# Optimization experiments

Measured on AMD Instinct MI355X. Metric: run time of the kernel, lower is better.

Reference implementation:

```python
import jax, jax.numpy as jnp
import numpy as np

H = 256  # hidden_dim
N = 500000  # num_orbitals
M = 8192  # num_molecules


def setup_inputs() -> dict:
    key = jax.random.key(0)
    ks = jax.random.split(key, 12)
    s = lambda fan_in: 1.0 / np.sqrt(fan_in)
    inp = {
        "orbital_embeddings": jax.random.normal(ks[0], (N, H), dtype=jnp.float32),
        "batch": jnp.sort(jax.random.randint(ks[1], (N,), 0, M, dtype=jnp.int32)),
        "num_molecules": M,
        # attention MLP: Linear(H, H//2) -> ReLU -> Linear(H//2, 1)
        "aW1": jax.random.uniform(ks[2], (H, H // 2), jnp.float32, -s(H), s(H)),
        "ab1": jnp.zeros((H // 2,), jnp.float32),
        "aW2": jax.random.uniform(ks[3], (H // 2, 1), jnp.float32, -s(H // 2), s(H // 2)),
        "ab2": jnp.zeros((1,), jnp.float32),
        # global head: Linear(H,H)->ReLU->Linear(H,H//2)->ReLU->Linear(H//2,1)
        "gW1": jax.random.uniform(ks[4], (H, H), jnp.float32, -s(H), s(H)),
        "gb1": jnp.zeros((H,), jnp.float32),
        "gW2": jax.random.uniform(ks[5], (H, H // 2), jnp.float32, -s(H), s(H)),
        "gb2": jnp.zeros((H // 2,), jnp.float32),
        "gW3": jax.random.uniform(ks[6], (H // 2, 1), jnp.float32, -s(H // 2), s(H // 2)),
        "gb3": jnp.zeros((1,), jnp.float32),
    }
    return inp


def reference(orbital_embeddings, batch, num_molecules, aW1, ab1, aW2, ab2,
              gW1, gb1, gW2, gb2, gW3, gb3):
    # attention logits: [N, 1] (dropout is identity in eval mode)
    h = jax.nn.relu(orbital_embeddings @ aW1 + ab1)
    logits = h @ aW2 + ab2  # [N, 1]

    # per-molecule (segment) softmax over orbitals, numerically stable
    lg = logits[:, 0]  # [N]
    seg_max = jax.ops.segment_max(lg, batch, num_segments=num_molecules)  # [M]
    seg_max = jnp.where(jnp.isfinite(seg_max), seg_max, 0.0)  # empty segments
    ex = jnp.exp(lg - seg_max[batch])  # [N]
    denom = jax.ops.segment_sum(ex, batch, num_segments=num_molecules)  # [M]
    w = ex / denom[batch]  # [N]

    # weighted scatter-add pooling -> [M, H]
    weighted = orbital_embeddings * w[:, None]
    mol = jax.ops.segment_sum(weighted, batch, num_segments=num_molecules)

    # global head MLP -> [M, 1]
    g = jax.nn.relu(mol @ gW1 + gb1)
    g = jax.nn.relu(g @ gW2 + gb2)
    return g @ gW3 + gb3
```

## Files before the change

kernel.cpp:

```cpp
#include <hip/hip_runtime.h>
#include <hip/hip_bf16.h>

#define H      256
#define CAP    64
#define GRID12 512

typedef _Float16 f16x8 __attribute__((ext_vector_type(8)));
typedef float    f32x4 __attribute__((ext_vector_type(4)));

#define AS3(p) ((__attribute__((address_space(3))) void*)(p))
#define AS1(p) ((const __attribute__((address_space(1))) void*)(p))

__global__ __launch_bounds__(256) void k0_pack(
    const float* __restrict__ aW1, const float* __restrict__ gW1,
    const float* __restrict__ gW2,
    _Float16* __restrict__ aW1F, float* __restrict__ gW1P, float* __restrict__ gW2P)
{
    int idx = blockIdx.x * 256 + threadIdx.x;
    int stride = gridDim.x * 256;
    for (int e8 = idx; e8 < 4096; e8 += stride) {
        int l = e8 & 63, kknt = e8 >> 6;
        int kk = kknt & 7, nt = kknt >> 3;
        int j = nt*16 + (l & 15);
        int kbase = kk*32 + (l >> 4)*8;
        f16x8 v;
        #pragma unroll
        for (int e = 0; e < 8; ++e) v[e] = (_Float16)aW1[(kbase + e)*128 + j];
        *reinterpret_cast<f16x8*>(aW1F + e8*8) = v;
    }
    for (int e = idx; e < 64*256*4; e += stride) {
        int s = e & 3, j = (e >> 2) & 255, kq = e >> 10;
        gW1P[e] = gW1[(kq*4+s)*256 + j];
    }
    for (int e = idx; e < 64*128*4; e += stride) {
        int s = e & 3, j = (e >> 2) & 127, kq = e >> 9;
        gW2P[e] = gW2[(kq*4+s)*128 + j];
    }
}

__global__ __launch_bounds__(256) void k2a_starts(
    const int* __restrict__ batch, int* __restrict__ starts, int N, int M)
{
    int i = blockIdx.x * 256 + threadIdx.x;
    if (i >= N) return;
    int b = batch[i];
    if (i == 0) {
        for (int m = 0; m <= b; ++m) starts[m] = 0;
    } else {
        int p = batch[i-1];
        for (int m = p + 1; m <= b; ++m) starts[m] = i;
    }
    if (i == N - 1) {
        for (int m = b + 1; m <= M; ++m) starts[m] = N;
    }
}

__global__ __launch_bounds__(256) void k12_fused(
    const float* __restrict__ emb, const int* __restrict__ starts,
    const _Float16* __restrict__ aW1F, const float* __restrict__ ab1,
    const float* __restrict__ aW2, const float* __restrict__ ab2,
    float* __restrict__ mol, int M)
{
    __shared__ __align__(16) float ef[CAP * H];
    __shared__ float pr[4][CAP];
    __shared__ float lgs[CAP];
    __shared__ float wl[CAP];

    const int t = threadIdx.x, w = t >> 6, l = t & 63;
    char* ldsb = reinterpret_cast<char*>(ef);
    const f32x4 zero = {0.f, 0.f, 0.f, 0.f};

    f16x8 bf[2][8];
    #pragma unroll
    for (int nt2 = 0; nt2 < 2; ++nt2)
        #pragma unroll
        for (int kk = 0; kk < 8; ++kk)
            bf[nt2][kk] = *reinterpret_cast<const f16x8*>(
                aW1F + (size_t)(((2*w + nt2)*8 + kk)*64 + l)*8);

    float b1v[2], w2v[2];
    #pragma unroll
    for (int nt2 = 0; nt2 < 2; ++nt2) {
        int j = 32*w + nt2*16 + (l & 15);
        b1v[nt2] = ab1[j];
        w2v[nt2] = aW2[j];
    }
    const float bo = ab2[0];

    int m = blockIdx.x, start = 0, end = 0;
    for (;;) {
        if (m >= M) return;
        start = starts[m]; end = starts[m + 1];
        if (start < end) break;
        mol[(size_t)m*H + t] = 0.f;
        m += GRID12;
    }

    int c0 = start;
    int cc = min(CAP, end - c0);
    float mx = -INFINITY, s = 0.f, acc = 0.f;

    for (;;) {
        const int  cur_m = m, cur_cc = cc;
        const bool last_chunk = (c0 + CAP >= end);

        __syncthreads();

        #pragma unroll
        for (int i = 0; i < 16; ++i) {
            int r = w*16 + i;
            if (r < cc) {
                const char* gs = reinterpret_cast<const char*>(emb + (size_t)(c0 + r)*H)
                               + ((l*16) ^ ((r & 7) << 4));
#if __has_builtin(__builtin_amdgcn_global_load_lds)
                __builtin_amdgcn_global_load_lds(AS1(gs), AS3(ldsb + r*1024), 16, 0, 0);
#else
                *reinterpret_cast<float4*>(ldsb + r*1024 + l*16) =
                    *reinterpret_cast<const float4*>(gs);
#endif
            }
        }

        int nm = m, nc0 = c0 + CAP, nend = end;
        bool have_next = true;
        if (last_chunk) {
            nm = m + GRID12;
            for (;;) {
                if (nm >= M) { have_next = false; break; }
                int ns = starts[nm], ne = starts[nm + 1];
                if (ns < ne) { nc0 = ns; nend = ne; break; }
                mol[(size_t)nm*H + t] = 0.f;
                nm += GRID12;
            }
        }
        int ncc = have_next ? min(CAP, nend - nc0) : 0;
        __syncthreads();

        const int nr = (cur_cc + 15) >> 4;
        for (int rt = 0; rt < nr; ++rt) {
            int row   = rt*16 + (l & 15);
            int rbase = row*1024 + (l >> 4)*32;
            int swz   = (row & 7) << 4;
            f32x4 a20 = zero, a21 = zero;
            #pragma unroll
            for (int kk = 0; kk < 8; ++kk) {
                int rb = rbase + kk*128;
                float4 a0 = *reinterpret_cast<const float4*>(ldsb + ( rb       ^ swz));
                float4 a1 = *reinterpret_cast<const float4*>(ldsb + ((rb + 16) ^ swz));
                f16x8 af;
                af[0]=(_Float16)a0.x; af[1]=(_Float16)a0.y; af[2]=(_Float16)a0.z; af[3]=(_Float16)a0.w;
                af[4]=(_Float16)a1.x; af[5]=(_Float16)a1.y; af[6]=(_Float16)a1.z; af[7]=(_Float16)a1.w;
                a20 = __builtin_amdgcn_mfma_f32_16x16x32_f16(af, bf[0][kk], a20, 0, 0, 0);
                a21 = __builtin_amdgcn_mfma_f32_16x16x32_f16(af, bf[1][kk], a21, 0, 0, 0);
            }
            #pragma unroll
            for (int r = 0; r < 4; ++r) {
                float h0 = a20[r] + b1v[0]; h0 = h0 > 0.f ? h0 : 0.f;
                float h1 = a21[r] + b1v[1]; h1 = h1 > 0.f ? h1 : 0.f;
                float p = h0*w2v[0] + h1*w2v[1];
                p += __shfl_xor(p, 1, 64);
                p += __shfl_xor(p, 2, 64);
                p += __shfl_xor(p, 4, 64);
                p += __shfl_xor(p, 8, 64);
                if ((l & 15) == 0) pr[w][rt*16 + (l >> 4)*4 + r] = p;
            }
        }
        __syncthreads();
        if (t < CAP) lgs[t] = pr[0][t] + pr[1][t] + pr[2][t] + pr[3][t] + bo;
        __syncthreads();

        float lg = (l < cur_cc) ? lgs[l] : -INFINITY;
        float mc = lg;
        mc = fmaxf(mc, __shfl_xor(mc, 1, 64));
        mc = fmaxf(mc, __shfl_xor(mc, 2, 64));
        mc = fmaxf(mc, __shfl_xor(mc, 4, 64));
        mc = fmaxf(mc, __shfl_xor(mc, 8, 64));
        mc = fmaxf(mc, __shfl_xor(mc, 16, 64));
        mc = fmaxf(mc, __shfl_xor(mc, 32, 64));
        float mxn = fmaxf(mx, mc);
        float rsc = __expf(mx - mxn);
        float e = (l < cur_cc) ? __expf(lg - mxn) : 0.f;
        float sc = e;
        sc += __shfl_xor(sc, 1, 64);
        sc += __shfl_xor(sc, 2, 64);
        sc += __shfl_xor(sc, 4, 64);
        sc += __shfl_xor(sc, 8, 64);
        sc += __shfl_xor(sc, 16, 64);
        sc += __shfl_xor(sc, 32, 64);
        s = s*rsc + sc;
        if (w == 0) wl[l] = e;
        mx = mxn;
        __syncthreads();

        acc *= rsc;
        #pragma unroll 4
        for (int g = 0; g < cur_cc; ++g) {
            float ev = *reinterpret_cast<const float*>(
                ldsb + ((g*1024 + t*4) ^ ((g & 7) << 4)));
            acc += wl[g] * ev;
        }

        if (last_chunk) {
            mol[(size_t)cur_m*H + t] = acc / s;
            mx = -INFINITY; s = 0.f; acc = 0.f;
        }
        if (!have_next) return;
        m = nm; c0 = nc0; end = nend; cc = ncc;
    }
}

__global__ __launch_bounds__(256) void k3_mlp(
    const float* __restrict__ mol, const float* __restrict__ gW1P,
    const float* __restrict__ gb1, const float* __restrict__ gW2P,
    const float* __restrict__ gb2, const float* __restrict__ gW3,
    const float* __restrict__ gb3, float* __restrict__ out, int M)
{
    __shared__ __align__(16) float mt[32 * 256];
    __shared__ __align__(16) float g1[32 * 256];
    __shared__ float tmp[4][16];
    int t = threadIdx.x;
    int blk = blockIdx.x;

    #pragma unroll
    for (int i = 0; i < 8; ++i) {
        int f = t + i*256;
        long gidx = (long)blk*2048 + f;
        float4 v = make_float4(0.f,0.f,0.f,0.f);
        if (gidx < (long)M*64) v = reinterpret_cast<const float4*>(mol)[gidx];
        reinterpret_cast<float4*>(mt)[f] = v;
    }
    __syncthreads();

    int j = t & 127, mh = t >> 7;

    float a0[16], a1[16];
    #pragma unroll
    for (int m = 0; m < 16; ++m) { a0[m] = 0.f; a1[m] = 0.f; }
    for (int kq = 0; kq < 64; ++kq) {
        float4 w0 = reinterpret_cast<const float4*>(gW1P)[kq*256 + j];
        float4 w1 = reinterpret_cast<const float4*>(gW1P)[kq*256 + j + 128];
        #pragma unroll
        for (int m = 0; m < 16; ++m) {
            float4 e = *reinterpret_cast<const float4*>(&mt[(mh*16 + m)*256 + kq*4]);
            a0[m] += e.x*w0.x + e.y*w0.y + e.z*w0.z + e.w*w0.w;
            a1[m] += e.x*w1.x + e.y*w1.y + e.z*w1.z + e.w*w1.w;
        }
    }
    {
        float b0 = gb1[j], b1 = gb1[j + 128];
        #pragma unroll
        for (int m = 0; m < 16; ++m) {
            float v0 = a0[m] + b0; v0 = v0 > 0.f ? v0 : 0.f;
            float v1 = a1[m] + b1; v1 = v1 > 0.f ? v1 : 0.f;
            g1[(mh*16 + m)*256 + j]       = v0;
            g1[(mh*16 + m)*256 + j + 128] = v1;
        }
    }
    __syncthreads();

    float a2[16];
    #pragma unroll
    for (int m = 0; m < 16; ++m) a2[m] = 0.f;
    for (int kq = 0; kq < 64; ++kq) {
        float4 w = reinterpret_cast<const float4*>(gW2P)[kq*128 + j];
        #pragma unroll
        for (int m = 0; m < 16; ++m) {
            float4 e = *reinterpret_cast<const float4*>(&g1[(mh*16 + m)*256 + kq*4]);
            a2[m] += e.x*w.x + e.y*w.y + e.z*w.z + e.w*w.w;
        }
    }

    float b2 = gb2[j], w3 = gW3[j];
    float p[16];
    #pragma unroll
    for (int m = 0; m < 16; ++m) {
        float v = a2[m] + b2; v = v > 0.f ? v : 0.f;
        p[m] = v * w3;
    }
    #pragma unroll
    for (int off = 32; off >= 1; off >>= 1) {
        #pragma unroll
        for (int m = 0; m < 16; ++m) p[m] += __shfl_xor(p[m], off, 64);
    }
    int wid = t >> 6;
    if ((t & 63) == 0) {
        #pragma unroll
        for (int m = 0; m < 16; ++m) tmp[wid][m] = p[m];
    }
    __syncthreads();
    if (t < 32) {
        int om = blk*32 + t;
        if (om < M) out[om] = tmp[(t >> 4)*2][t & 15] + tmp[(t >> 4)*2 + 1][t & 15] + gb3[0];
    }
}

extern "C" void kernel_launch(void* const* d_in, const int* in_sizes, int n_in,
                              void* d_out, int out_size, void* d_ws, size_t ws_size,
                              hipStream_t stream) {
    const float* emb  = (const float*)d_in[0];
    const int*   batch= (const int*)d_in[1];
    const float* aW1  = (const float*)d_in[3];
    const float* ab1  = (const float*)d_in[4];
    const float* aW2  = (const float*)d_in[5];
    const float* ab2  = (const float*)d_in[6];
    const float* gW1  = (const float*)d_in[7];
    const float* gb1  = (const float*)d_in[8];
    const float* gW2  = (const float*)d_in[9];
    const float* gb2  = (const float*)d_in[10];
    const float* gW3  = (const float*)d_in[11];
    const float* gb3  = (const float*)d_in[12];
    float* outp = (float*)d_out;

    int N = in_sizes[0] / H;
    int M = out_size;

    char* ws = (char*)d_ws;
    size_t off = 0;
    float*     mol    = (float*)(ws + off);    off += (8u<<20);
    _Float16*  aW1F   = (_Float16*)(ws + off); off += 65536;
    float*     gW1P   = (float*)(ws + off);    off += 262144;
    float*     gW2P   = (float*)(ws + off);    off += 131072;
    int*       starts = (int*)(ws + off);      off += (size_t)(M+1)*4;

    int g12 = M < GRID12 ? M : GRID12;

    k0_pack<<<64, 256, 0, stream>>>(aW1, gW1, gW2, aW1F, gW1P, gW2P);
    k2a_starts<<<(N + 255)/256, 256, 0, stream>>>(batch, starts, N, M);
    k12_fused<<<g12, 256, 0, stream>>>(emb, starts, aW1F, ab1, aW2, ab2, mol, M);
    k3_mlp<<<(M + 31)/32, 256, 0, stream>>>(mol, gW1P, gb1, gW2P, gb2, gW3, gb3, outp, M);
}
```

Measured before the change: 254.0 us.

## Double-buffer embedding chunks in LDS to prefetch the next chunk during compute

The fused attention-pool kernel now keeps two LDS buffers of 32 rows each instead of one 64-row buffer. While the current chunk is processed, the global_load_lds for the next chunk (or next molecule) is issued, and partial waits via s_waitcnt vmcnt plus raw s_barrier replace several __syncthreads. The intent is to hide global-memory latency behind the MFMA and softmax work. It also drops the separate lgs reduction step and clamps out-of-range rows to the last valid row instead of skipping them. Smaller chunks add more per-chunk barrier and softmax overhead, and the hand-placed waitcnt handling is fragile.

After: 276.2 us. 1.09x slower.

```diff
diff --git a/kernel.cpp b/kernel.cpp
--- a/kernel.cpp
+++ b/kernel.cpp
@@ -2,14 +2,21 @@
 #include <hip/hip_bf16.h>
 
 #define H      256
-#define CAP    64
+#define CAP    32
 #define GRID12 512
+#define RPW    8
 
 typedef _Float16 f16x8 __attribute__((ext_vector_type(8)));
 typedef float    f32x4 __attribute__((ext_vector_type(4)));
 
 #define AS3(p) ((__attribute__((address_space(3))) void*)(p))
 #define AS1(p) ((const __attribute__((address_space(1))) void*)(p))
+
+#define VMWAIT8() asm volatile("s_waitcnt vmcnt(8)" ::: "memory")
+#define VMWAIT0() asm volatile("s_waitcnt vmcnt(0)" ::: "memory")
+#define LGKM0()   asm volatile("s_waitcnt lgkmcnt(0)" ::: "memory")
+#define SBAR()    __builtin_amdgcn_s_barrier()
+#define SCHED0()  __builtin_amdgcn_sched_barrier(0)
 
 __global__ __launch_bounds__(256) void k0_pack(
     const float* __restrict__ aW1, const float* __restrict__ gW1,
@@ -61,13 +68,11 @@
     const float* __restrict__ aW2, const float* __restrict__ ab2,
     float* __restrict__ mol, int M)
 {
-    __shared__ __align__(16) float ef[CAP * H];
+    __shared__ __align__(16) float ef[2][CAP * H];
     __shared__ float pr[4][CAP];
-    __shared__ float lgs[CAP];
     __shared__ float wl[CAP];
 
     const int t = threadIdx.x, w = t >> 6, l = t & 63;
-    char* ldsb = reinterpret_cast<char*>(ef);
     const f32x4 zero = {0.f, 0.f, 0.f, 0.f};
 
     f16x8 bf[2][8];
@@ -98,28 +103,25 @@
 
     int c0 = start;
     int cc = min(CAP, end - c0);
+
+#define ISSUE8(BUF, C0, CC) do {                                                 \
+    char* dst_ = reinterpret_cast<char*>(ef[BUF]);                               \
+    _Pragma("unroll")                                                            \
+    for (int i_ = 0; i_ < RPW; ++i_) {                                           \
+        int r_  = w*RPW + i_;                                                    \
+        int rr_ = r_ < (CC) ? r_ : (CC) - 1;                                     \
+        const char* gs_ = reinterpret_cast<const char*>(                         \
+            emb + (size_t)((C0) + rr_)*H) + ((l*16) ^ ((rr_ & 7) << 4));         \
+        __builtin_amdgcn_global_load_lds(AS1(gs_), AS3(dst_ + r_*1024), 16, 0, 0);\
+    } } while (0)
+
+    ISSUE8(0, c0, cc);
+    int cur = 0;
     float mx = -INFINITY, s = 0.f, acc = 0.f;
 
     for (;;) {
         const int  cur_m = m, cur_cc = cc;
         const bool last_chunk = (c0 + CAP >= end);
-
-        __syncthreads();
-
-        #pragma unroll
-        for (int i = 0; i < 16; ++i) {
-            int r = w*16 + i;
-            if (r < cc) {
-                const char* gs = reinterpret_cast<const char*>(emb + (size_t)(c0 + r)*H)
-                               + ((l*16) ^ ((r & 7) << 4));
-#if __has_builtin(__builtin_amdgcn_global_load_lds)
-                __builtin_amdgcn_global_load_lds(AS1(gs), AS3(ldsb + r*1024), 16, 0, 0);
-#else
-                *reinterpret_cast<float4*>(ldsb + r*1024 + l*16) =
-                    *reinterpret_cast<const float4*>(gs);
-#endif
-            }
-        }
 
         int nm = m, nc0 = c0 + CAP, nend = end;
         bool have_next = true;
@@ -134,7 +136,19 @@
             }
         }
         int ncc = have_next ? min(CAP, nend - nc0) : 0;
-        __syncthreads();
+
+        SBAR();
+
+        if (have_next) {
+            ISSUE8(cur ^ 1, nc0, ncc);
+            VMWAIT8();
+        } else {
+            VMWAIT0();
+        }
+        SCHED0();
+        SBAR();
+
+        const char* bufb = reinterpret_cast<const char*>(ef[cur]);
 
         const int nr = (cur_cc + 15) >> 4;
         for (int rt = 0; rt < nr; ++rt) {
@@ -145,8 +159,8 @@
             #pragma unroll
             for (int kk = 0; kk < 8; ++kk) {
                 int rb = rbase + kk*128;
-                float4 a0 = *reinterpret_cast<const float4*>(ldsb + ( rb       ^ swz));
-                float4 a1 = *reinterpret_cast<const float4*>(ldsb + ((rb + 16) ^ swz));
+                float4 a0 = *reinterpret_cast<const float4*>(bufb + ( rb       ^ swz));
+                float4 a1 = *reinterpret_cast<const float4*>(bufb + ((rb + 16) ^ swz));
                 f16x8 af;
                 af[0]=(_Float16)a0.x; af[1]=(_Float16)a0.y; af[2]=(_Float16)a0.z; af[3]=(_Float16)a0.w;
                 af[4]=(_Float16)a1.x; af[5]=(_Float16)a1.y; af[6]=(_Float16)a1.z; af[7]=(_Float16)a1.w;
@@ -165,11 +179,11 @@
                 if ((l & 15) == 0) pr[w][rt*16 + (l >> 4)*4 + r] = p;
             }
         }
-        __syncthreads();
-        if (t < CAP) lgs[t] = pr[0][t] + pr[1][t] + pr[2][t] + pr[3][t] + bo;
-        __syncthreads();
-
-        float lg = (l < cur_cc) ? lgs[l] : -INFINITY;
+        LGKM0(); SCHED0();
+        SBAR();
+
+        float lg = -INFINITY;
+        if (l < cur_cc) lg = pr[0][l] + pr[1][l] + pr[2][l] + pr[3][l] + bo;
         float mc = lg;
         mc = fmaxf(mc, __shfl_xor(mc, 1, 64));
         mc = fmaxf(mc, __shfl_xor(mc, 2, 64));
@@ -188,15 +202,16 @@
         sc += __shfl_xor(sc, 16, 64);
         sc += __shfl_xor(sc, 32, 64);
         s = s*rsc + sc;
-        if (w == 0) wl[l] = e;
         mx = mxn;
-        __syncthreads();
+        if (w == 0 && l < CAP) wl[l] = e;
+        LGKM0(); SCHED0();
+        SBAR();
 
         acc *= rsc;
-        #pragma unroll 4
+        #pragma unroll 8
         for (int g = 0; g < cur_cc; ++g) {
             float ev = *reinterpret_cast<const float*>(
-                ldsb + ((g*1024 + t*4) ^ ((g & 7) << 4)));
+                bufb + ((g*1024 + t*4) ^ ((g & 7) << 4)));
             acc += wl[g] * ev;
         }
 
@@ -206,7 +221,9 @@
         }
         if (!have_next) return;
         m = nm; c0 = nc0; end = nend; cc = ncc;
-    }
+        cur ^= 1;
+    }
+#undef ISSUE8
 }
 
 __global__ __launch_bounds__(256) void k3_mlp(
```

## Halve segment chunk size to raise occupancy and simplify per-molecule loop

Applied to the files above, without the earlier changes.

The orbital chunk staged in LDS shrinks from 64 to 32 rows, halving the main shared buffer. The launch bound now asks for 4 blocks per CU and the grid size is doubled. The lookahead logic that peeked at the next molecule's range is replaced by a plain nested loop over molecules and chunks. Row loads are clamped so every wave always issues its fixed set of loads, and the tile loops are fully unrolled. The aim is to hide global-load latency through more resident waves. In exchange, each molecule now needs more chunks, and so more barriers and online-softmax rescale steps.

Measured after the change: 364.7 us. +43.6%, slower.

```diff
diff --git a/kernel.cpp b/kernel.cpp
--- a/kernel.cpp
+++ b/kernel.cpp
@@ -2,8 +2,9 @@
 #include <hip/hip_bf16.h>
 
 #define H      256
-#define CAP    64
-#define GRID12 512
+#define CAP    32
+#define GRID12 1024
+#define RPW    8
 
 typedef _Float16 f16x8 __attribute__((ext_vector_type(8)));
 typedef float    f32x4 __attribute__((ext_vector_type(4)));
@@ -55,7 +56,7 @@
     }
 }
 
-__global__ __launch_bounds__(256) void k12_fused(
+__global__ __launch_bounds__(256, 4) void k12_fused(
     const float* __restrict__ emb, const int* __restrict__ starts,
     const _Float16* __restrict__ aW1F, const float* __restrict__ ab1,
     const float* __restrict__ aW2, const float* __restrict__ ab2,
@@ -63,7 +64,6 @@
 {
     __shared__ __align__(16) float ef[CAP * H];
     __shared__ float pr[4][CAP];
-    __shared__ float lgs[CAP];
     __shared__ float wl[CAP];
 
     const int t = threadIdx.x, w = t >> 6, l = t & 63;
@@ -87,31 +87,23 @@
     }
     const float bo = ab2[0];
 
-    int m = blockIdx.x, start = 0, end = 0;
-    for (;;) {
-        if (m >= M) return;
-        start = starts[m]; end = starts[m + 1];
-        if (start < end) break;
-        mol[(size_t)m*H + t] = 0.f;
-        m += GRID12;
-    }
-
-    int c0 = start;
-    int cc = min(CAP, end - c0);
-    float mx = -INFINITY, s = 0.f, acc = 0.f;
-
-    for (;;) {
-        const int  cur_m = m, cur_cc = cc;
-        const bool last_chunk = (c0 + CAP >= end);
-
-        __syncthreads();
-
-        #pragma unroll
-        for (int i = 0; i < 16; ++i) {
-            int r = w*16 + i;
-            if (r < cc) {
-                const char* gs = reinterpret_cast<const char*>(emb + (size_t)(c0 + r)*H)
-                               + ((l*16) ^ ((r & 7) << 4));
+    for (int m = blockIdx.x; m < M; m += GRID12) {
+        const int start = starts[m], end = starts[m + 1];
+        if (start >= end) { mol[(size_t)m*H + t] = 0.f; continue; }
+
+        float mx = -INFINITY, s = 0.f, acc = 0.f;
+
+        for (int c0 = start; c0 < end; c0 += CAP) {
+            const int cc = min(CAP, end - c0);
+
+            __syncthreads();
+
+            #pragma unroll
+            for (int i = 0; i < RPW; ++i) {
+                int r  = w*RPW + i;
+                int rr = r < cc ? r : cc - 1;
+                const char* gs = reinterpret_cast<const char*>(emb + (size_t)(c0 + rr)*H)
+                               + ((l*16) ^ ((rr & 7) << 4));
 #if __has_builtin(__builtin_amdgcn_global_load_lds)
                 __builtin_amdgcn_global_load_lds(AS1(gs), AS3(ldsb + r*1024), 16, 0, 0);
 #else
@@ -119,93 +111,72 @@
                     *reinterpret_cast<const float4*>(gs);
 #endif
             }
-        }
-
-        int nm = m, nc0 = c0 + CAP, nend = end;
-        bool have_next = true;
-        if (last_chunk) {
-            nm = m + GRID12;
-            for (;;) {
-                if (nm >= M) { have_next = false; break; }
-                int ns = starts[nm], ne = starts[nm + 1];
-                if (ns < ne) { nc0 = ns; nend = ne; break; }
-                mol[(size_t)nm*H + t] = 0.f;
-                nm += GRID12;
+            __syncthreads();
+
+            #pragma unroll
+            for (int rt = 0; rt < 2; ++rt) {
+                int row   = rt*16 + (l & 15);
+                int rbase = row*1024 + (l >> 4)*32;
+                int swz   = (row & 7) << 4;
+                f32x4 a20 = zero, a21 = zero;
+                #pragma unroll
+                for (int kk = 0; kk < 8; ++kk) {
+                    int rb = rbase + kk*128;
+                    float4 a0 = *reinterpret_cast<const float4*>(ldsb + ( rb       ^ swz));
+                    float4 a1 = *reinterpret_cast<const float4*>(ldsb + ((rb + 16) ^ swz));
+                    f16x8 af;
+                    af[0]=(_Float16)a0.x; af[1]=(_Float16)a0.y; af[2]=(_Float16)a0.z; af[3]=(_Float16)a0.w;
+                    af[4]=(_Float16)a1.x; af[5]=(_Float16)a1.y; af[6]=(_Float16)a1.z; af[7]=(_Float16)a1.w;
+                    a20 = __builtin_amdgcn_mfma_f32_16x16x32_f16(af, bf[0][kk], a20, 0, 0, 0);
+                    a21 = __builtin_amdgcn_mfma_f32_16x16x32_f16(af, bf[1][kk], a21, 0, 0, 0);
+                }
+                #pragma unroll
+                for (int r = 0; r < 4; ++r) {
+                    float h0 = a20[r] + b1v[0]; h0 = h0 > 0.f ? h0 : 0.f;
+                    float h1 = a21[r] + b1v[1]; h1 = h1 > 0.f ? h1 : 0.f;
+                    float p = h0*w2v[0] + h1*w2v[1];
+                    p += __shfl_xor(p, 1, 64);
+                    p += __shfl_xor(p, 2, 64);
+                    p += __shfl_xor(p, 4, 64);
+                    p += __shfl_xor(p, 8, 64);
+                    if ((l & 15) == 0) pr[w][rt*16 + (l >> 4)*4 + r] = p;
+                }
+            }
+            __syncthreads();
+
+            float lg = -INFINITY;
+            if (l < cc) lg = pr[0][l] + pr[1][l] + pr[2][l] + pr[3][l] + bo;
+            float mc = lg;
+            mc = fmaxf(mc, __shfl_xor(mc, 1, 64));
+            mc = fmaxf(mc, __shfl_xor(mc, 2, 64));
+            mc = fmaxf(mc, __shfl_xor(mc, 4, 64));
+            mc = fmaxf(mc, __shfl_xor(mc, 8, 64));
+            mc = fmaxf(mc, __shfl_xor(mc, 16, 64));
+            mc = fmaxf(mc, __shfl_xor(mc, 32, 64));
+            float mxn = fmaxf(mx, mc);
+            float rsc = __expf(mx - mxn);
+            float e = (l < cc) ? __expf(lg - mxn) : 0.f;
+            float sc = e;
+            sc += __shfl_xor(sc, 1, 64);
+            sc += __shfl_xor(sc, 2, 64);
+            sc += __shfl_xor(sc, 4, 64);
+            sc += __shfl_xor(sc, 8, 64);
+            sc += __shfl_xor(sc, 16, 64);
+            sc += __shfl_xor(sc, 32, 64);
+            s = s*rsc + sc;
+            mx = mxn;
+            if (w == 0 && l < CAP) wl[l] = e;
+            __syncthreads();
+
+            acc *= rsc;
+            #pragma unroll
+            for (int g = 0; g < CAP; ++g) {
+                float ev = *reinterpret_cast<const float*>(
+                    ldsb + ((g*1024 + t*4) ^ ((g & 7) << 4)));
+                acc += wl[g] * ev;
             }
         }
-        int ncc = have_next ? min(CAP, nend - nc0) : 0;
-        __syncthreads();
-
-        const int nr = (cur_cc + 15) >> 4;
-        for (int rt = 0; rt < nr; ++rt) {
-            int row   = rt*16 + (l & 15);
-            int rbase = row*1024 + (l >> 4)*32;
-            int swz   = (row & 7) << 4;
-            f32x4 a20 = zero, a21 = zero;
-            #pragma unroll
-            for (int kk = 0; kk < 8; ++kk) {
-                int rb = rbase + kk*128;
-                float4 a0 = *reinterpret_cast<const float4*>(ldsb + ( rb       ^ swz));
-                float4 a1 = *reinterpret_cast<const float4*>(ldsb + ((rb + 16) ^ swz));
-                f16x8 af;
-                af[0]=(_Float16)a0.x; af[1]=(_Float16)a0.y; af[2]=(_Float16)a0.z; af[3]=(_Float16)a0.w;
-                af[4]=(_Float16)a1.x; af[5]=(_Float16)a1.y; af[6]=(_Float16)a1.z; af[7]=(_Float16)a1.w;
-                a20 = __builtin_amdgcn_mfma_f32_16x16x32_f16(af, bf[0][kk], a20, 0, 0, 0);
-                a21 = __builtin_amdgcn_mfma_f32_16x16x32_f16(af, bf[1][kk], a21, 0, 0, 0);
-            }
-            #pragma unroll
-            for (int r = 0; r < 4; ++r) {
-                float h0 = a20[r] + b1v[0]; h0 = h0 > 0.f ? h0 : 0.f;
-                float h1 = a21[r] + b1v[1]; h1 = h1 > 0.f ? h1 : 0.f;
-                float p = h0*w2v[0] + h1*w2v[1];
-                p += __shfl_xor(p, 1, 64);
-                p += __shfl_xor(p, 2, 64);
-                p += __shfl_xor(p, 4, 64);
-                p += __shfl_xor(p, 8, 64);
-                if ((l & 15) == 0) pr[w][rt*16 + (l >> 4)*4 + r] = p;
-            }
-        }
-        __syncthreads();
-        if (t < CAP) lgs[t] = pr[0][t] + pr[1][t] + pr[2][t] + pr[3][t] + bo;
-        __syncthreads();
-
-        float lg = (l < cur_cc) ? lgs[l] : -INFINITY;
-        float mc = lg;
-        mc = fmaxf(mc, __shfl_xor(mc, 1, 64));
-        mc = fmaxf(mc, __shfl_xor(mc, 2, 64));
-        mc = fmaxf(mc, __shfl_xor(mc, 4, 64));
-        mc = fmaxf(mc, __shfl_xor(mc, 8, 64));
-        mc = fmaxf(mc, __shfl_xor(mc, 16, 64));
-        mc = fmaxf(mc, __shfl_xor(mc, 32, 64));
-        float mxn = fmaxf(mx, mc);
-        float rsc = __expf(mx - mxn);
-        float e = (l < cur_cc) ? __expf(lg - mxn) : 0.f;
-        float sc = e;
-        sc += __shfl_xor(sc, 1, 64);
-        sc += __shfl_xor(sc, 2, 64);
-        sc += __shfl_xor(sc, 4, 64);
-        sc += __shfl_xor(sc, 8, 64);
-        sc += __shfl_xor(sc, 16, 64);
-        sc += __shfl_xor(sc, 32, 64);
-        s = s*rsc + sc;
-        if (w == 0) wl[l] = e;
-        mx = mxn;
-        __syncthreads();
-
-        acc *= rsc;
-        #pragma unroll 4
-        for (int g = 0; g < cur_cc; ++g) {
-            float ev = *reinterpret_cast<const float*>(
-                ldsb + ((g*1024 + t*4) ^ ((g & 7) << 4)));
-            acc += wl[g] * ev;
-        }
-
-        if (last_chunk) {
-            mol[(size_t)cur_m*H + t] = acc / s;
-            mx = -INFINITY; s = 0.f; acc = 0.f;
-        }
-        if (!have_next) return;
-        m = nm; c0 = nc0; end = nend; cc = ncc;
+        mol[(size_t)m*H + t] = acc / s;
     }
 }
 
```
